# Kernel optimization log

Hardware: AMD Instinct MI355X
Metric: run time of the kernel (lower is better)

Reference implementation:

```python
import jax, jax.numpy as jnp
import numpy as np

B, S, D, F_INT = 8, 1024, 1024, 4096
N_EDGES = 262144
NUM_REL = 2
LN_EPS = 1e-6


def setup_inputs() -> dict:
    key = jax.random.key(0)
    ks = jax.random.split(key, 10)
    N = B * S
    glorot_w = float(np.sqrt(6.0 / (D + F_INT)))
    glorot_r = float(np.sqrt(6.0 / (D + F_INT)))
    return {
        "hidden_states": jax.random.normal(ks[0], (B, S, D), dtype=jnp.float32),
        "weight": jax.random.uniform(ks[1], (NUM_REL, D, F_INT), jnp.float32, -glorot_w, glorot_w),
        "root": jax.random.uniform(ks[2], (D, F_INT), jnp.float32, -glorot_r, glorot_r),
        "bias": jnp.zeros((F_INT,), jnp.float32),
        "wo": jax.random.normal(ks[3], (F_INT, D), dtype=jnp.float32) * 0.02,
        "ln_gamma": jnp.ones((D,), jnp.float32),
        "ln_beta": jnp.zeros((D,), jnp.float32),
        "edge_index": jax.random.randint(ks[4], (2, N_EDGES), 0, N, dtype=jnp.int32),
        "edge_type": jax.random.randint(ks[5], (N_EDGES,), 0, NUM_REL, dtype=jnp.int32),
    }


def reference(hidden_states, weight, root, bias, wo, ln_gamma, ln_beta, edge_index, edge_type):
    Bz, Sq, Dm = hidden_states.shape
    N = Bz * Sq
    # LayerNorm
    mu = hidden_states.mean(-1, keepdims=True)
    var = jnp.mean((hidden_states - mu) ** 2, axis=-1, keepdims=True)
    norm_x = (hidden_states - mu) * jax.lax.rsqrt(var + LN_EPS) * ln_gamma + ln_beta
    x = norm_x.reshape(N, Dm)  # [N, D] node features

    src, dst = edge_index[0], edge_index[1]
    out = jnp.zeros((N, weight.shape[2]), dtype=x.dtype)
    # RGCNConv: per-relation masked gather -> scatter-mean -> matmul
    for r in range(NUM_REL):
        mask = (edge_type == r)
        msg = jnp.where(mask[:, None], x[src], 0.0)          # [E, D]
        agg = jax.ops.segment_sum(msg, dst, num_segments=N)  # [N, D]
        cnt = jax.ops.segment_sum(mask.astype(x.dtype), dst, num_segments=N)
        h = agg / jnp.maximum(cnt, 1.0)[:, None]             # mean aggr (0 if no edges)
        out = out + h @ weight[r]
    out = out + x @ root + bias
    # relu -> wo -> residual (dropout = identity at eval)
    out = jax.nn.relu(out) @ wo
    return hidden_states + out.reshape(Bz, Sq, Dm)
```

## Files before the change

kernel.cpp:

```cpp
#include <hip/hip_runtime.h>


typedef unsigned short u16;
typedef unsigned int   u32;
typedef __attribute__((ext_vector_type(8))) short bf16x8;
typedef __attribute__((ext_vector_type(4))) float f32x4;
typedef __attribute__((ext_vector_type(2))) float f32x2;

#define E_NUM  262144
#define NNODE  8192
#define NBKT   (2 * NNODE)
#define DDIM   1024
#define FDIM   4096
#define KCAT   3072
#define LN_EPS 1e-6f

struct alignas(8) u16x4 { u16 x, y, z, w; };

__device__ __forceinline__ u16 f2bf(float f) {
  u32 u = __float_as_uint(f);
  u32 r = u + 0x7fffu + ((u >> 16) & 1u);
  return (u16)(r >> 16);
}
__device__ __forceinline__ float bf2f(u16 h) {
  return __uint_as_float(((u32)h) << 16);
}

__device__ __forceinline__ u32 enc_fp8_1(float f) {
  u32 u = __float_as_uint(f);
  u32 s = u >> 31;
  u32 mag = u & 0x7fffffffu;
  mag = mag + 0x7ffffu + ((mag >> 20) & 1u);
  if (mag > 0x43e00000u) mag = 0x43e00000u;
  u32 e = mag >> 23;
  return (e <= 120u) ? 0u
                     : ((s << 7) | ((e - 120u) << 3) | ((mag >> 20) & 7u));
}

__device__ __forceinline__ u32 pack4_fp8(float a, float b, float c, float d) {
#if __has_builtin(__builtin_amdgcn_cvt_pk_fp8_f32)
  int v = 0;
  v = __builtin_amdgcn_cvt_pk_fp8_f32(a, b, v, false);
  v = __builtin_amdgcn_cvt_pk_fp8_f32(c, d, v, true);
  return (u32)v;
#else
  return enc_fp8_1(a) | (enc_fp8_1(b) << 8) | (enc_fp8_1(c) << 16) |
         (enc_fp8_1(d) << 24);
#endif
}

__device__ __forceinline__ float dec_fp8_1(u32 b) {
  u32 e = (b >> 3) & 15u;
  u32 f = ((b & 0x80u) << 24) | ((e + 120u) << 23) | ((b & 7u) << 20);
  return e ? __uint_as_float(f) : 0.0f;
}

__device__ __forceinline__ void acc4_fp8(float* a, u32 q) {
#if __has_builtin(__builtin_amdgcn_cvt_pk_f32_fp8)
  f32x2 p0 = __builtin_amdgcn_cvt_pk_f32_fp8((int)q, false);
  f32x2 p1 = __builtin_amdgcn_cvt_pk_f32_fp8((int)q, true);
  a[0] += p0.x; a[1] += p0.y; a[2] += p1.x; a[3] += p1.y;
#else
  a[0] += dec_fp8_1(q);       a[1] += dec_fp8_1(q >> 8);
  a[2] += dec_fp8_1(q >> 16); a[3] += dec_fp8_1(q >> 24);
#endif
}

#define GLD16(gp, lp)                                              \
  __builtin_amdgcn_global_load_lds(                                \
      (__attribute__((address_space(1))) u32*)(gp),                \
      (__attribute__((address_space(3))) u32*)(lp), 16, 0, 0)

__global__ void ln_kernel(const float* __restrict__ hs,
                          const float* __restrict__ gamma,
                          const float* __restrict__ beta,
                          u16* __restrict__ hcat,
                          u32* __restrict__ xq) {
  const int row = blockIdx.x;
  const int tid = threadIdx.x;
  const float4 v = ((const float4*)(hs + (size_t)row * DDIM))[tid];

  __shared__ float r1[256], r2[256];
  r1[tid] = v.x + v.y + v.z + v.w;
  r2[tid] = v.x * v.x + v.y * v.y + v.z * v.z + v.w * v.w;
  __syncthreads();
  for (int st = 128; st > 0; st >>= 1) {
    if (tid < st) { r1[tid] += r1[tid + st]; r2[tid] += r2[tid + st]; }
    __syncthreads();
  }
  const float mean = r1[0] * (1.0f / DDIM);
  const float var  = r2[0] * (1.0f / DDIM) - mean * mean;
  const float rs   = rsqrtf(var + LN_EPS);

  const int base = tid * 4;
  const float4 g = *(const float4*)(gamma + base);
  const float4 b = *(const float4*)(beta + base);
  const float o0 = (v.x - mean) * rs * g.x + b.x;
  const float o1 = (v.y - mean) * rs * g.y + b.y;
  const float o2 = (v.z - mean) * rs * g.z + b.z;
  const float o3 = (v.w - mean) * rs * g.w + b.w;
  u16x4 o;
  o.x = f2bf(o0); o.y = f2bf(o1); o.z = f2bf(o2); o.w = f2bf(o3);
  *(u16x4*)(hcat + (size_t)row * KCAT + 2048 + base) = o;
  xq[row * 256 + tid] = pack4_fp8(o0, o1, o2, o3);
}

__global__ void cvt_transpose(const float* __restrict__ srcA,
                              const float* __restrict__ srcB,
                              int splitK, int K, int N,
                              u16* __restrict__ dst) {
  __shared__ float tile[32][33];
  const int n0 = blockIdx.x * 32, k0 = blockIdx.y * 32;
  const int tx = threadIdx.x, ty = threadIdx.y;
  for (int i = ty; i < 32; i += 8) {
    const int k = k0 + i;
    const float v = (k < splitK) ? srcA[(size_t)k * N + n0 + tx]
                                 : srcB[(size_t)(k - splitK) * N + n0 + tx];
    tile[i][tx] = v;
  }
  __syncthreads();
  for (int i = ty; i < 32; i += 8) {
    dst[(size_t)(n0 + i) * K + k0 + tx] = f2bf(tile[tx][i]);
  }
}

__global__ void count_kernel(const int* __restrict__ edge_index,
                             const int* __restrict__ edge_type,
                             int* __restrict__ cnt) {
  const int e = blockIdx.x * 256 + threadIdx.x;
  const int d = edge_index[E_NUM + e];
  const int r = edge_type[e];
  atomicAdd(&cnt[r * NNODE + d], 1);
}

__global__ __launch_bounds__(1024) void scan_kernel(const int* __restrict__ cnt,
                                                    int* __restrict__ off,
                                                    int* __restrict__ cursor) {
  __shared__ int partial[1024];
  const int tid  = threadIdx.x;
  const int base = tid * 16;
  int local[16];
  int s = 0;
#pragma unroll
  for (int i = 0; i < 16; ++i) { local[i] = s; s += cnt[base + i]; }
  partial[tid] = s;
  __syncthreads();
  for (int st = 1; st < 1024; st <<= 1) {
    const int v = (tid >= st) ? partial[tid - st] : 0;
    __syncthreads();
    partial[tid] += v;
    __syncthreads();
  }
  const int pre = (tid == 0) ? 0 : partial[tid - 1];
#pragma unroll
  for (int i = 0; i < 16; ++i) {
    const int o = pre + local[i];
    off[base + i]    = o;
    cursor[base + i] = o;
  }
}

__global__ void fill_kernel(const int* __restrict__ edge_index,
                            const int* __restrict__ edge_type,
                            int* __restrict__ cursor,
                            int* __restrict__ bucket_src) {
  const int e = blockIdx.x * 256 + threadIdx.x;
  const int s = edge_index[e];
  const int d = edge_index[E_NUM + e];
  const int r = edge_type[e];
  const int pos = atomicAdd(&cursor[r * NNODE + d], 1);
  bucket_src[pos] = s;
}

__global__ __launch_bounds__(256) void aggregate_kernel(
    const int* __restrict__ cnt, const int* __restrict__ off,
    const int* __restrict__ bucket_src, const u32* __restrict__ xq,
    u16* __restrict__ hcat) {
  const int b    = blockIdx.x;
  const int r    = b >> 13;
  const int node = b & (NNODE - 1);
  const int tid  = threadIdx.x;
  const int g    = tid >> 6;
  const int c    = tid & 63;
  const int n     = cnt[b];
  const int start = off[b];

  __shared__ int   ids[256];
  __shared__ float red[3 * 1024];
  float a[16] = {};

  for (int c0 = 0; c0 < n; c0 += 256) {
    const int m = min(n - c0, 256);
    __syncthreads();
    if (tid < m) ids[tid] = bucket_src[start + c0 + tid];
    __syncthreads();
    int j = g;
    for (; j + 4 < m; j += 8) {
      const int s0 = ids[j], s1 = ids[j + 4];
      const uint4 x0 = *(const uint4*)(xq + s0 * 256 + c * 4);
      const uint4 x1 = *(const uint4*)(xq + s1 * 256 + c * 4);
      acc4_fp8(a + 0,  x0.x); acc4_fp8(a + 4,  x0.y);
      acc4_fp8(a + 8,  x0.z); acc4_fp8(a + 12, x0.w);
      acc4_fp8(a + 0,  x1.x); acc4_fp8(a + 4,  x1.y);
      acc4_fp8(a + 8,  x1.z); acc4_fp8(a + 12, x1.w);
    }
    for (; j < m; j += 4) {
      const int s0 = ids[j];
      const uint4 x0 = *(const uint4*)(xq + s0 * 256 + c * 4);
      acc4_fp8(a + 0,  x0.x); acc4_fp8(a + 4,  x0.y);
      acc4_fp8(a + 8,  x0.z); acc4_fp8(a + 12, x0.w);
    }
  }

  if (g != 0) {
    float* d = red + (g - 1) * 1024 + c * 16;
#pragma unroll
    for (int i = 0; i < 4; ++i)
      *(float4*)(d + i * 4) = make_float4(a[i*4+0], a[i*4+1], a[i*4+2], a[i*4+3]);
  }
  __syncthreads();
  if (g == 0) {
#pragma unroll
    for (int k = 0; k < 3; ++k) {
      const float* d = red + k * 1024 + c * 16;
#pragma unroll
      for (int i = 0; i < 16; ++i) a[i] += d[i];
    }
    const float inv = 1.0f / fmaxf((float)n, 1.0f);
    uint4 o0, o1;
    o0.x = (u32)f2bf(a[0] * inv)  | ((u32)f2bf(a[1] * inv)  << 16);
    o0.y = (u32)f2bf(a[2] * inv)  | ((u32)f2bf(a[3] * inv)  << 16);
    o0.z = (u32)f2bf(a[4] * inv)  | ((u32)f2bf(a[5] * inv)  << 16);
    o0.w = (u32)f2bf(a[6] * inv)  | ((u32)f2bf(a[7] * inv)  << 16);
    o1.x = (u32)f2bf(a[8] * inv)  | ((u32)f2bf(a[9] * inv)  << 16);
    o1.y = (u32)f2bf(a[10] * inv) | ((u32)f2bf(a[11] * inv) << 16);
    o1.z = (u32)f2bf(a[12] * inv) | ((u32)f2bf(a[13] * inv) << 16);
    o1.w = (u32)f2bf(a[14] * inv) | ((u32)f2bf(a[15] * inv) << 16);
    u16* dp = hcat + (size_t)node * KCAT + (size_t)r * DDIM + c * 16;
    *(uint4*)(dp)     = o0;
    *(uint4*)(dp + 8) = o1;
  }
}


#define MF16(a, b, c) __builtin_amdgcn_mfma_f32_16x16x32_bf16(a, b, c, 0, 0, 0)

#define STAGE_A(t, p, b)                                                   \
  { GLD16(gA0 + (size_t)(t) * 64 + (size_t)(p) * KP,                       \
          &sA[b][(p) * 8192 + lofs0]);                                     \
    GLD16(gA1 + (size_t)(t) * 64 + (size_t)(p) * KP,                       \
          &sA[b][(p) * 8192 + lofs1]); }

#define STAGE_B(t, p, b)                                                   \
  { GLD16(gB0 + (size_t)(t) * 64 + (size_t)(p) * KP,                       \
          &sB[b][(p) * 8192 + lofs0]);                                     \
    GLD16(gB1 + (size_t)(t) * 64 + (size_t)(p) * KP,                       \
          &sB[b][(p) * 8192 + lofs1]); }

#define BVLOAD(b)                                                          \
  { const bf16x8* pB_ = (const bf16x8*)sB[b];                              \
    bv[0][0] = pB_[brow80 + sega0]; bv[0][1] = pB_[brow80 + sega1];        \
    bv[1][0] = pB_[brow81 + sega0]; bv[1][1] = pB_[brow81 + sega1];        \
    bv[2][0] = pB_[brow82 + sega0]; bv[2][1] = pB_[brow82 + sega1];        \
    bv[3][0] = pB_[brow83 + sega0]; bv[3][1] = pB_[brow83 + sega1]; }

#define NOWAIT ((void)0)
#define NOSTAGE ((void)0)
#define VM4 asm volatile("s_waitcnt vmcnt(4)" ::: "memory")
#define VM2 asm volatile("s_waitcnt vmcnt(2)" ::: "memory")
#define VM0 asm volatile("s_waitcnt vmcnt(0)" ::: "memory")

#define PHASE(Q, BUFI, STAGE, ENDW)                                        \
  { const bf16x8* pA_ = (const bf16x8*)sA[BUFI];                           \
    bf16x8 a00 = pA_[arow8[2 * (Q)] + sega0];                              \
    bf16x8 a01 = pA_[arow8[2 * (Q)] + sega1];                              \
    bf16x8 a10 = pA_[arow8[2 * (Q) + 1] + sega0];                          \
    bf16x8 a11 = pA_[arow8[2 * (Q) + 1] + sega1];                          \
    STAGE;                                                                 \
    __builtin_amdgcn_s_barrier();                                          \
    asm volatile("s_waitcnt lgkmcnt(0)" ::: "memory");                     \
    __builtin_amdgcn_s_setprio(1);                                         \
    _Pragma("unroll")                                                      \
    for (int ni = 0; ni < 4; ++ni) {                                       \
      acc[2 * (Q)][ni]     = MF16(a00, bv[ni][0], acc[2 * (Q)][ni]);       \
      acc[2 * (Q)][ni]     = MF16(a01, bv[ni][1], acc[2 * (Q)][ni]);       \
      acc[2 * (Q) + 1][ni] = MF16(a10, bv[ni][0], acc[2 * (Q) + 1][ni]);   \
      acc[2 * (Q) + 1][ni] = MF16(a11, bv[ni][1], acc[2 * (Q) + 1][ni]);   \
    }                                                                      \
    __builtin_amdgcn_s_setprio(0);                                         \
    ENDW;                                                                  \
    __builtin_amdgcn_s_barrier(); }

__global__ __launch_bounds__(512) void gemm1_kernel(
    const u16* __restrict__ A, const u16* __restrict__ Bt,
    const float* __restrict__ bias, u16* __restrict__ obf) {
  const int K = KCAT, N = FDIM;
  const int NT = K / 64;
  const size_t KP = (size_t)128 * K;
  __shared__ __align__(16) u16 sA[2][16384];
  __shared__ __align__(16) u16 sB[2][16384];

  const int tid  = threadIdx.x;
  const int lane = tid & 63;
  const int wave = tid >> 6;
  const int wr = wave >> 2, wc = wave & 3;
  const int lr = lane & 15, quad = lane >> 4;

  const int bid = blockIdx.x;
  const int swz = (bid & 7) * 64 + (bid >> 3);
  const int bm = (swz >> 4) * 256;
  const int bn = (swz & 15) * 256;

  int lofs0, lofs1;
  const u16 *gA0, *gA1, *gB0, *gB1;
  {
    const int s0 = tid,       r0 = s0 >> 3, g0 = (s0 & 7) ^ (r0 & 7);
    const int s1 = tid + 512, r1 = s1 >> 3, g1 = (s1 & 7) ^ (r1 & 7);
    gA0 = A  + (size_t)(bm + r0) * K + g0 * 8;
    gA1 = A  + (size_t)(bm + r1) * K + g1 * 8;
    gB0 = Bt + (size_t)(bn + r0) * K + g0 * 8;
    gB1 = Bt + (size_t)(bn + r1) * K + g1 * 8;
    lofs0 = s0 * 8; lofs1 = s1 * 8;
  }

  int arow8[8];
#pragma unroll
  for (int mi = 0; mi < 8; ++mi) arow8[mi] = (wr * 128 + mi * 16 + lr) * 8;
  const int brow80 = (wc * 64 +  0 + lr) * 8;
  const int brow81 = (wc * 64 + 16 + lr) * 8;
  const int brow82 = (wc * 64 + 32 + lr) * 8;
  const int brow83 = (wc * 64 + 48 + lr) * 8;
  const int sega0 = quad ^ (lr & 7);
  const int sega1 = (4 + quad) ^ (lr & 7);

  f32x4 acc[8][4] = {};
  bf16x8 bv[4][2];

  STAGE_B(0, 0, 0) STAGE_B(0, 1, 0)
  STAGE_A(0, 0, 0) STAGE_A(0, 1, 0)
  STAGE_B(1, 0, 1) STAGE_B(1, 1, 1)
  asm volatile("s_waitcnt vmcnt(4)" ::: "memory");
  __builtin_amdgcn_s_barrier();

  for (int tt = 0; tt < NT - 2; tt += 2) {
    PHASE(0, 0, BVLOAD(0); STAGE_A(tt + 1, 0, 1), NOWAIT)
    PHASE(1, 0, STAGE_A(tt + 1, 1, 1), NOWAIT)
    PHASE(2, 0, STAGE_B(tt + 2, 0, 0), NOWAIT)
    PHASE(3, 0, STAGE_B(tt + 2, 1, 0), VM4)
    PHASE(0, 1, BVLOAD(1); STAGE_A(tt + 2, 0, 0), NOWAIT)
    PHASE(1, 1, STAGE_A(tt + 2, 1, 0), NOWAIT)
    PHASE(2, 1, STAGE_B(tt + 3, 0, 1), NOWAIT)
    PHASE(3, 1, STAGE_B(tt + 3, 1, 1), VM4)
  }
  PHASE(0, 0, BVLOAD(0); STAGE_A(NT - 1, 0, 1), NOWAIT)
  PHASE(1, 0, STAGE_A(NT - 1, 1, 1), NOWAIT)
  PHASE(2, 0, NOSTAGE, NOWAIT)
  PHASE(3, 0, NOSTAGE, VM0)
  PHASE(0, 1, BVLOAD(1), NOWAIT)
  PHASE(1, 1, NOSTAGE, NOWAIT)
  PHASE(2, 1, NOSTAGE, NOWAIT)
  PHASE(3, 1, NOSTAGE, NOWAIT)

#pragma unroll
  for (int mi = 0; mi < 8; ++mi) {
#pragma unroll
    for (int ni = 0; ni < 4; ++ni) {
      const int col  = bn + wc * 64 + ni * 16 + lr;
      const int row0 = bm + wr * 128 + mi * 16 + quad * 4;
      const float bb = bias[col];
#pragma unroll
      for (int r = 0; r < 4; ++r) {
        float v = acc[mi][ni][r] + bb;
        v = fmaxf(v, 0.0f);
        obf[(size_t)(row0 + r) * N + col] = f2bf(v);
      }
    }
  }
}

__global__ __launch_bounds__(512) void gemm2_kernel(
    const u16* __restrict__ A, const u16* __restrict__ Bt,
    const float* __restrict__ resid, float* __restrict__ out) {
  const int K = FDIM, N = DDIM;
  const int NT = K / 64;
  const size_t KP = (size_t)128 * K;
  __shared__ __align__(16) u16 sA[2][16384];
  __shared__ __align__(16) u16 sB[2][8192];

  const int tid  = threadIdx.x;
  const int lane = tid & 63;
  const int wave = tid >> 6;
  const int wr = wave >> 1, wc = wave & 1;
  const int lr = lane & 15, quad = lane >> 4;

  const int bid = blockIdx.x;
  const int swz = (bid & 7) * 32 + (bid >> 3);
  const int bm = (swz >> 3) * 256;
  const int bn = (swz & 7) * 128;

  int lofs0, lofs1;
  const u16 *gA0, *gA1, *gB0, *gB1;
  {
    const int s0 = tid,       r0 = s0 >> 3, g0 = (s0 & 7) ^ (r0 & 7);
    const int s1 = tid + 512, r1 = s1 >> 3, g1 = (s1 & 7) ^ (r1 & 7);
    gA0 = A  + (size_t)(bm + r0) * K + g0 * 8;
    gA1 = A  + (size_t)(bm + r1) * K + g1 * 8;
    gB0 = Bt + (size_t)(bn + r0) * K + g0 * 8;
    gB1 = Bt + (size_t)(bn + r1) * K + g1 * 8;
    lofs0 = s0 * 8; lofs1 = s1 * 8;
  }

  int arow8[4];
#pragma unroll
  for (int mi = 0; mi < 4; ++mi) arow8[mi] = (wr * 64 + mi * 16 + lr) * 8;
  const int brow80 = (wc * 64 +  0 + lr) * 8;
  const int brow81 = (wc * 64 + 16 + lr) * 8;
  const int brow82 = (wc * 64 + 32 + lr) * 8;
  const int brow83 = (wc * 64 + 48 + lr) * 8;
  const int sega0 = quad ^ (lr & 7);
  const int sega1 = (4 + quad) ^ (lr & 7);

  f32x4 acc[4][4] = {};
  bf16x8 bv[4][2];

  STAGE_B(0, 0, 0)
  STAGE_A(0, 0, 0) STAGE_A(0, 1, 0)
  STAGE_B(1, 0, 1)
  asm volatile("s_waitcnt vmcnt(2)" ::: "memory");
  __builtin_amdgcn_s_barrier();

  for (int tt = 0; tt < NT - 2; tt += 2) {
    PHASE(0, 0, BVLOAD(0); STAGE_A(tt + 1, 0, 1), NOWAIT)
    PHASE(1, 0, STAGE_A(tt + 1, 1, 1); STAGE_B(tt + 2, 0, 0), VM2)
    PHASE(0, 1, BVLOAD(1); STAGE_A(tt + 2, 0, 0), NOWAIT)
    PHASE(1, 1, STAGE_A(tt + 2, 1, 0); STAGE_B(tt + 3, 0, 1), VM2)
  }
  PHASE(0, 0, BVLOAD(0); STAGE_A(NT - 1, 0, 1), NOWAIT)
  PHASE(1, 0, STAGE_A(NT - 1, 1, 1), VM0)
  PHASE(0, 1, BVLOAD(1), NOWAIT)
  PHASE(1, 1, NOSTAGE, NOWAIT)

#pragma unroll
  for (int mi = 0; mi < 4; ++mi) {
#pragma unroll
    for (int ni = 0; ni < 4; ++ni) {
      const int col  = bn + wc * 64 + ni * 16 + lr;
      const int row0 = bm + wr * 64 + mi * 16 + quad * 4;
#pragma unroll
      for (int r = 0; r < 4; ++r) {
        const size_t idx = (size_t)(row0 + r) * N + col;
        out[idx] = resid[idx] + acc[mi][ni][r];
      }
    }
  }
}

extern "C" void kernel_launch(void* const* d_in, const int* in_sizes, int n_in,
                              void* d_out, int out_size, void* d_ws, size_t ws_size,
                              hipStream_t stream) {
  const float* hs     = (const float*)d_in[0];
  const float* weight = (const float*)d_in[1];
  const float* root   = (const float*)d_in[2];
  const float* bias   = (const float*)d_in[3];
  const float* wo     = (const float*)d_in[4];
  const float* gamma  = (const float*)d_in[5];
  const float* beta   = (const float*)d_in[6];
  const int* edge_index = (const int*)d_in[7];
  const int* edge_type  = (const int*)d_in[8];
  float* out = (float*)d_out;

  char* ws = (char*)d_ws;
  u16*   hcat       = (u16*)(ws + 0);
  u16*   WcatT      = (u16*)(ws + 50331648);
  u16*   woT        = (u16*)(ws + 75497472);
  u16*   out1       = (u16*)(ws + 83886080);
  int*   bucket_src = (int*)(ws + 83886080);
  int*   cnt        = (int*)(ws + 84934656);
  int*   off        = (int*)(ws + 85000192);
  int*   cursor     = (int*)(ws + 85065728);
  u32*   xq         = (u32*)(ws + 85131264);

  (void)hipMemsetAsync(cnt, 0, 65536, stream);

  ln_kernel<<<NNODE, 256, 0, stream>>>(hs, gamma, beta, hcat, xq);

  cvt_transpose<<<dim3(FDIM / 32, KCAT / 32), dim3(32, 8), 0, stream>>>(
      weight, root, 2048, KCAT, FDIM, WcatT);
  cvt_transpose<<<dim3(DDIM / 32, FDIM / 32), dim3(32, 8), 0, stream>>>(
      wo, wo, FDIM, FDIM, DDIM, woT);

  count_kernel<<<E_NUM / 256, 256, 0, stream>>>(edge_index, edge_type, cnt);
  scan_kernel<<<1, 1024, 0, stream>>>(cnt, off, cursor);
  fill_kernel<<<E_NUM / 256, 256, 0, stream>>>(edge_index, edge_type, cursor, bucket_src);
  aggregate_kernel<<<NBKT, 256, 0, stream>>>(cnt, off, bucket_src, xq, hcat);

  gemm1_kernel<<<512, 512, 0, stream>>>(hcat, WcatT, bias, out1);

  gemm2_kernel<<<256, 512, 0, stream>>>(out1, woT, hs, out);
}
```

Baseline: 474.5 us.

## Use one wavefront per bucket in aggregation and double-buffer A fragments in GEMM1

The aggregation kernel now gives each (relation, node) bucket to a single 64-lane wavefront, four buckets per block. Source ids are broadcast with shuffles instead of staged through LDS, which removes the shared-memory cross-wave reduction and its syncthreads. Separately, the GEMM1 main loop now uses two register banks of A fragments and prefetches the next phase's A reads after the barrier, ahead of the current MFMAs, with sched_barrier and setprio fencing. The intent is to hide LDS read latency behind matrix math. In exchange, register pressure rises and aggregation parallelism per bucket falls, since there are fewer lanes per node.

```diff
diff --git a/kernel.cpp b/kernel.cpp
--- a/kernel.cpp
+++ b/kernel.cpp
@@ -64,6 +64,11 @@
   a[0] += dec_fp8_1(q);       a[1] += dec_fp8_1(q >> 8);
   a[2] += dec_fp8_1(q >> 16); a[3] += dec_fp8_1(q >> 24);
 #endif
+}
+
+__device__ __forceinline__ void acc16_fp8(float* a, uint4 x) {
+  acc4_fp8(a + 0,  x.x); acc4_fp8(a + 4,  x.y);
+  acc4_fp8(a + 8,  x.z); acc4_fp8(a + 12, x.w);
 }
 
 #define GLD16(gp, lp)                                              \
@@ -176,70 +181,51 @@
     const int* __restrict__ cnt, const int* __restrict__ off,
     const int* __restrict__ bucket_src, const u32* __restrict__ xq,
     u16* __restrict__ hcat) {
-  const int b    = blockIdx.x;
+  const int b    = blockIdx.x * 4 + (threadIdx.x >> 6);
+  const int lane = threadIdx.x & 63;
   const int r    = b >> 13;
   const int node = b & (NNODE - 1);
-  const int tid  = threadIdx.x;
-  const int g    = tid >> 6;
-  const int c    = tid & 63;
   const int n     = cnt[b];
   const int start = off[b];
 
-  __shared__ int   ids[256];
-  __shared__ float red[3 * 1024];
   float a[16] = {};
 
-  for (int c0 = 0; c0 < n; c0 += 256) {
-    const int m = min(n - c0, 256);
-    __syncthreads();
-    if (tid < m) ids[tid] = bucket_src[start + c0 + tid];
-    __syncthreads();
-    int j = g;
-    for (; j + 4 < m; j += 8) {
-      const int s0 = ids[j], s1 = ids[j + 4];
-      const uint4 x0 = *(const uint4*)(xq + s0 * 256 + c * 4);
-      const uint4 x1 = *(const uint4*)(xq + s1 * 256 + c * 4);
-      acc4_fp8(a + 0,  x0.x); acc4_fp8(a + 4,  x0.y);
-      acc4_fp8(a + 8,  x0.z); acc4_fp8(a + 12, x0.w);
-      acc4_fp8(a + 0,  x1.x); acc4_fp8(a + 4,  x1.y);
-      acc4_fp8(a + 8,  x1.z); acc4_fp8(a + 12, x1.w);
+  for (int j0 = 0; j0 < n; j0 += 64) {
+    const int m = min(n - j0, 64);
+    const int myid = (lane < m) ? bucket_src[start + j0 + lane] : 0;
+    int j = 0;
+    for (; j + 3 < m; j += 4) {
+      const int s0 = __shfl(myid, j,     64);
+      const int s1 = __shfl(myid, j + 1, 64);
+      const int s2 = __shfl(myid, j + 2, 64);
+      const int s3 = __shfl(myid, j + 3, 64);
+      const uint4 x0 = *(const uint4*)(xq + s0 * 256 + lane * 4);
+      const uint4 x1 = *(const uint4*)(xq + s1 * 256 + lane * 4);
+      const uint4 x2 = *(const uint4*)(xq + s2 * 256 + lane * 4);
+      const uint4 x3 = *(const uint4*)(xq + s3 * 256 + lane * 4);
+      acc16_fp8(a, x0); acc16_fp8(a, x1);
+      acc16_fp8(a, x2); acc16_fp8(a, x3);
     }
-    for (; j < m; j += 4) {
-      const int s0 = ids[j];
-      const uint4 x0 = *(const uint4*)(xq + s0 * 256 + c * 4);
-      acc4_fp8(a + 0,  x0.x); acc4_fp8(a + 4,  x0.y);
-      acc4_fp8(a + 8,  x0.z); acc4_fp8(a + 12, x0.w);
+    for (; j < m; ++j) {
+      const int s0 = __shfl(myid, j, 64);
+      const uint4 x0 = *(const uint4*)(xq + s0 * 256 + lane * 4);
+      acc16_fp8(a, x0);
     }
   }
 
-  if (g != 0) {
-    float* d = red + (g - 1) * 1024 + c * 16;
-#pragma unroll
-    for (int i = 0; i < 4; ++i)
-      *(float4*)(d + i * 4) = make_float4(a[i*4+0], a[i*4+1], a[i*4+2], a[i*4+3]);
-  }
-  __syncthreads();
-  if (g == 0) {
-#pragma unroll
-    for (int k = 0; k < 3; ++k) {
-      const float* d = red + k * 1024 + c * 16;
-#pragma unroll
-      for (int i = 0; i < 16; ++i) a[i] += d[i];
-    }
-    const float inv = 1.0f / fmaxf((float)n, 1.0f);
-    uint4 o0, o1;
-    o0.x = (u32)f2bf(a[0] * inv)  | ((u32)f2bf(a[1] * inv)  << 16);
-    o0.y = (u32)f2bf(a[2] * inv)  | ((u32)f2bf(a[3] * inv)  << 16);
-    o0.z = (u32)f2bf(a[4] * inv)  | ((u32)f2bf(a[5] * inv)  << 16);
-    o0.w = (u32)f2bf(a[6] * inv)  | ((u32)f2bf(a[7] * inv)  << 16);
-    o1.x = (u32)f2bf(a[8] * inv)  | ((u32)f2bf(a[9] * inv)  << 16);
-    o1.y = (u32)f2bf(a[10] * inv) | ((u32)f2bf(a[11] * inv) << 16);
-    o1.z = (u32)f2bf(a[12] * inv) | ((u32)f2bf(a[13] * inv) << 16);
-    o1.w = (u32)f2bf(a[14] * inv) | ((u32)f2bf(a[15] * inv) << 16);
-    u16* dp = hcat + (size_t)node * KCAT + (size_t)r * DDIM + c * 16;
-    *(uint4*)(dp)     = o0;
-    *(uint4*)(dp + 8) = o1;
-  }
+  const float inv = 1.0f / fmaxf((float)n, 1.0f);
+  uint4 o0, o1;
+  o0.x = (u32)f2bf(a[0] * inv)  | ((u32)f2bf(a[1] * inv)  << 16);
+  o0.y = (u32)f2bf(a[2] * inv)  | ((u32)f2bf(a[3] * inv)  << 16);
+  o0.z = (u32)f2bf(a[4] * inv)  | ((u32)f2bf(a[5] * inv)  << 16);
+  o0.w = (u32)f2bf(a[6] * inv)  | ((u32)f2bf(a[7] * inv)  << 16);
+  o1.x = (u32)f2bf(a[8] * inv)  | ((u32)f2bf(a[9] * inv)  << 16);
+  o1.y = (u32)f2bf(a[10] * inv) | ((u32)f2bf(a[11] * inv) << 16);
+  o1.z = (u32)f2bf(a[12] * inv) | ((u32)f2bf(a[13] * inv) << 16);
+  o1.w = (u32)f2bf(a[14] * inv) | ((u32)f2bf(a[15] * inv) << 16);
+  u16* dp = hcat + (size_t)node * KCAT + (size_t)r * DDIM + lane * 16;
+  *(uint4*)(dp)     = o0;
+  *(uint4*)(dp + 8) = o1;
 }
 
 
@@ -266,9 +252,39 @@
 
 #define NOWAIT ((void)0)
 #define NOSTAGE ((void)0)
+#define NOOP ((void)0)
 #define VM4 asm volatile("s_waitcnt vmcnt(4)" ::: "memory")
 #define VM2 asm volatile("s_waitcnt vmcnt(2)" ::: "memory")
 #define VM0 asm volatile("s_waitcnt vmcnt(0)" ::: "memory")
+
+#define AREAD(BANK, Q, BUFI)                                               \
+  { const bf16x8* pA_ = (const bf16x8*)sA[BUFI];                           \
+    af##BANK##0 = pA_[arow8[2 * (Q)] + sega0];                             \
+    af##BANK##1 = pA_[arow8[2 * (Q)] + sega1];                             \
+    af##BANK##2 = pA_[arow8[2 * (Q) + 1] + sega0];                         \
+    af##BANK##3 = pA_[arow8[2 * (Q) + 1] + sega1]; }
+
+#define AMFMA(BANK, Q)                                                     \
+    _Pragma("unroll")                                                      \
+    for (int ni = 0; ni < 4; ++ni) {                                       \
+      acc[2 * (Q)][ni]     = MF16(af##BANK##0, bv[ni][0], acc[2 * (Q)][ni]);\
+      acc[2 * (Q)][ni]     = MF16(af##BANK##1, bv[ni][1], acc[2 * (Q)][ni]);\
+      acc[2 * (Q) + 1][ni] = MF16(af##BANK##2, bv[ni][0], acc[2 * (Q) + 1][ni]);\
+      acc[2 * (Q) + 1][ni] = MF16(af##BANK##3, bv[ni][1], acc[2 * (Q) + 1][ni]);\
+    }
+
+#define PHX(Q, BANK, OWN, PRE, STAGE, ENDW)                                \
+  { OWN;                                                                   \
+    STAGE;                                                                 \
+    __builtin_amdgcn_s_barrier();                                          \
+    asm volatile("s_waitcnt lgkmcnt(0)" ::: "memory");                     \
+    PRE;                                                                   \
+    __builtin_amdgcn_sched_barrier(0);                                     \
+    __builtin_amdgcn_s_setprio(1);                                         \
+    AMFMA(BANK, Q)                                                         \
+    __builtin_amdgcn_s_setprio(0);                                         \
+    ENDW;                                                                  \
+    __builtin_amdgcn_s_barrier(); }
 
 #define PHASE(Q, BUFI, STAGE, ENDW)                                        \
   { const bf16x8* pA_ = (const bf16x8*)sA[BUFI];                           \
@@ -335,6 +351,8 @@
 
   f32x4 acc[8][4] = {};
   bf16x8 bv[4][2];
+  bf16x8 af00, af01, af02, af03;
+  bf16x8 af10, af11, af12, af13;
 
   STAGE_B(0, 0, 0) STAGE_B(0, 1, 0)
   STAGE_A(0, 0, 0) STAGE_A(0, 1, 0)
@@ -343,23 +361,23 @@
   __builtin_amdgcn_s_barrier();
 
   for (int tt = 0; tt < NT - 2; tt += 2) {
-    PHASE(0, 0, BVLOAD(0); STAGE_A(tt + 1, 0, 1), NOWAIT)
-    PHASE(1, 0, STAGE_A(tt + 1, 1, 1), NOWAIT)
-    PHASE(2, 0, STAGE_B(tt + 2, 0, 0), NOWAIT)
-    PHASE(3, 0, STAGE_B(tt + 2, 1, 0), VM4)
-    PHASE(0, 1, BVLOAD(1); STAGE_A(tt + 2, 0, 0), NOWAIT)
-    PHASE(1, 1, STAGE_A(tt + 2, 1, 0), NOWAIT)
-    PHASE(2, 1, STAGE_B(tt + 3, 0, 1), NOWAIT)
-    PHASE(3, 1, STAGE_B(tt + 3, 1, 1), VM4)
-  }
-  PHASE(0, 0, BVLOAD(0); STAGE_A(NT - 1, 0, 1), NOWAIT)
-  PHASE(1, 0, STAGE_A(NT - 1, 1, 1), NOWAIT)
-  PHASE(2, 0, NOSTAGE, NOWAIT)
-  PHASE(3, 0, NOSTAGE, VM0)
-  PHASE(0, 1, BVLOAD(1), NOWAIT)
-  PHASE(1, 1, NOSTAGE, NOWAIT)
-  PHASE(2, 1, NOSTAGE, NOWAIT)
-  PHASE(3, 1, NOSTAGE, NOWAIT)
+    PHX(0, 0, AREAD(0, 0, 0); BVLOAD(0), AREAD(1, 1, 0), STAGE_A(tt + 1, 0, 1), NOWAIT)
+    PHX(1, 1, NOOP,                      AREAD(0, 2, 0), STAGE_A(tt + 1, 1, 1), NOWAIT)
+    PHX(2, 0, NOOP,                      AREAD(1, 3, 0), STAGE_B(tt + 2, 0, 0), NOWAIT)
+    PHX(3, 1, NOOP,                      NOOP,           STAGE_B(tt + 2, 1, 0), VM4)
+    PHX(0, 0, AREAD(0, 0, 1); BVLOAD(1), AREAD(1, 1, 1), STAGE_A(tt + 2, 0, 0), NOWAIT)
+    PHX(1, 1, NOOP,                      AREAD(0, 2, 1), STAGE_A(tt + 2, 1, 0), NOWAIT)
+    PHX(2, 0, NOOP,                      AREAD(1, 3, 1), STAGE_B(tt + 3, 0, 1), NOWAIT)
+    PHX(3, 1, NOOP,                      NOOP,           STAGE_B(tt + 3, 1, 1), VM4)
+  }
+  PHX(0, 0, AREAD(0, 0, 0); BVLOAD(0), AREAD(1, 1, 0), STAGE_A(NT - 1, 0, 1), NOWAIT)
+  PHX(1, 1, NOOP,                      AREAD(0, 2, 0), STAGE_A(NT - 1, 1, 1), NOWAIT)
+  PHX(2, 0, NOOP,                      AREAD(1, 3, 0), NOSTAGE, NOWAIT)
+  PHX(3, 1, NOOP,                      NOOP,           NOSTAGE, VM0)
+  PHX(0, 0, AREAD(0, 0, 1); BVLOAD(1), AREAD(1, 1, 1), NOSTAGE, NOWAIT)
+  PHX(1, 1, NOOP,                      AREAD(0, 2, 1), NOSTAGE, NOWAIT)
+  PHX(2, 0, NOOP,                      AREAD(1, 3, 1), NOSTAGE, NOWAIT)
+  PHX(3, 1, NOOP,                      NOOP,           NOSTAGE, NOWAIT)
 
 #pragma unroll
   for (int mi = 0; mi < 8; ++mi) {
@@ -492,7 +510,7 @@
   count_kernel<<<E_NUM / 256, 256, 0, stream>>>(edge_index, edge_type, cnt);
   scan_kernel<<<1, 1024, 0, stream>>>(cnt, off, cursor);
   fill_kernel<<<E_NUM / 256, 256, 0, stream>>>(edge_index, edge_type, cursor, bucket_src);
-  aggregate_kernel<<<NBKT, 256, 0, stream>>>(cnt, off, bucket_src, xq, hcat);
+  aggregate_kernel<<<NBKT / 4, 256, 0, stream>>>(cnt, off, bucket_src, xq, hcat);
 
   gemm1_kernel<<<512, 512, 0, stream>>>(hcat, WcatT, bias, out1);
 
```

Result: no change. 483.3 us (+1.9%).

## Fuse edge counting into LayerNorm, use wave-per-bucket aggregation, stage GEMM1 epilogue via LDS

Applied to the files above, without the earlier changes.

The edge-count atomics now run inside the LayerNorm kernel, so the separate count kernel is gone. Aggregation maps one wavefront to each (relation, node) bucket and broadcasts source ids with shuffles. This removes the LDS id staging, the cross-wave reduction and the block barriers. The GEMM1 epilogue writes bias+ReLU bf16 results into reused shared memory, then emits coalesced 16-byte row stores instead of scattered 2-byte stores. It adds two extra barriers per half tile, and each bucket's gather now runs on a single wave.

```diff
diff --git a/kernel.cpp b/kernel.cpp
--- a/kernel.cpp
+++ b/kernel.cpp
@@ -66,6 +66,11 @@
 #endif
 }
 
+__device__ __forceinline__ void acc16_fp8(float* a, uint4 x) {
+  acc4_fp8(a + 0,  x.x); acc4_fp8(a + 4,  x.y);
+  acc4_fp8(a + 8,  x.z); acc4_fp8(a + 12, x.w);
+}
+
 #define GLD16(gp, lp)                                              \
   __builtin_amdgcn_global_load_lds(                                \
       (__attribute__((address_space(1))) u32*)(gp),                \
@@ -75,10 +80,20 @@
                           const float* __restrict__ gamma,
                           const float* __restrict__ beta,
                           u16* __restrict__ hcat,
-                          u32* __restrict__ xq) {
+                          u32* __restrict__ xq,
+                          const int* __restrict__ edge_index,
+                          const int* __restrict__ edge_type,
+                          int* __restrict__ cnt) {
   const int row = blockIdx.x;
   const int tid = threadIdx.x;
   const float4 v = ((const float4*)(hs + (size_t)row * DDIM))[tid];
+
+  if (tid < 32) {
+    const int e = (row << 5) + tid;
+    const int d = edge_index[E_NUM + e];
+    const int r = edge_type[e];
+    atomicAdd(&cnt[r * NNODE + d], 1);
+  }
 
   __shared__ float r1[256], r2[256];
   r1[tid] = v.x + v.y + v.z + v.w;
@@ -124,15 +139,6 @@
   }
 }
 
-__global__ void count_kernel(const int* __restrict__ edge_index,
-                             const int* __restrict__ edge_type,
-                             int* __restrict__ cnt) {
-  const int e = blockIdx.x * 256 + threadIdx.x;
-  const int d = edge_index[E_NUM + e];
-  const int r = edge_type[e];
-  atomicAdd(&cnt[r * NNODE + d], 1);
-}
-
 __global__ __launch_bounds__(1024) void scan_kernel(const int* __restrict__ cnt,
                                                     int* __restrict__ off,
                                                     int* __restrict__ cursor) {
@@ -176,70 +182,51 @@
     const int* __restrict__ cnt, const int* __restrict__ off,
     const int* __restrict__ bucket_src, const u32* __restrict__ xq,
     u16* __restrict__ hcat) {
-  const int b    = blockIdx.x;
+  const int b    = blockIdx.x * 4 + (threadIdx.x >> 6);
+  const int lane = threadIdx.x & 63;
   const int r    = b >> 13;
   const int node = b & (NNODE - 1);
-  const int tid  = threadIdx.x;
-  const int g    = tid >> 6;
-  const int c    = tid & 63;
   const int n     = cnt[b];
   const int start = off[b];
 
-  __shared__ int   ids[256];
-  __shared__ float red[3 * 1024];
   float a[16] = {};
 
-  for (int c0 = 0; c0 < n; c0 += 256) {
-    const int m = min(n - c0, 256);
-    __syncthreads();
-    if (tid < m) ids[tid] = bucket_src[start + c0 + tid];
-    __syncthreads();
-    int j = g;
-    for (; j + 4 < m; j += 8) {
-      const int s0 = ids[j], s1 = ids[j + 4];
-      const uint4 x0 = *(const uint4*)(xq + s0 * 256 + c * 4);
-      const uint4 x1 = *(const uint4*)(xq + s1 * 256 + c * 4);
-      acc4_fp8(a + 0,  x0.x); acc4_fp8(a + 4,  x0.y);
-      acc4_fp8(a + 8,  x0.z); acc4_fp8(a + 12, x0.w);
-      acc4_fp8(a + 0,  x1.x); acc4_fp8(a + 4,  x1.y);
-      acc4_fp8(a + 8,  x1.z); acc4_fp8(a + 12, x1.w);
+  for (int j0 = 0; j0 < n; j0 += 64) {
+    const int m = min(n - j0, 64);
+    const int myid = (lane < m) ? bucket_src[start + j0 + lane] : 0;
+    int j = 0;
+    for (; j + 3 < m; j += 4) {
+      const int s0 = __shfl(myid, j,     64);
+      const int s1 = __shfl(myid, j + 1, 64);
+      const int s2 = __shfl(myid, j + 2, 64);
+      const int s3 = __shfl(myid, j + 3, 64);
+      const uint4 x0 = *(const uint4*)(xq + s0 * 256 + lane * 4);
+      const uint4 x1 = *(const uint4*)(xq + s1 * 256 + lane * 4);
+      const uint4 x2 = *(const uint4*)(xq + s2 * 256 + lane * 4);
+      const uint4 x3 = *(const uint4*)(xq + s3 * 256 + lane * 4);
+      acc16_fp8(a, x0); acc16_fp8(a, x1);
+      acc16_fp8(a, x2); acc16_fp8(a, x3);
     }
-    for (; j < m; j += 4) {
-      const int s0 = ids[j];
-      const uint4 x0 = *(const uint4*)(xq + s0 * 256 + c * 4);
-      acc4_fp8(a + 0,  x0.x); acc4_fp8(a + 4,  x0.y);
-      acc4_fp8(a + 8,  x0.z); acc4_fp8(a + 12, x0.w);
+    for (; j < m; ++j) {
+      const int s0 = __shfl(myid, j, 64);
+      const uint4 x0 = *(const uint4*)(xq + s0 * 256 + lane * 4);
+      acc16_fp8(a, x0);
     }
   }
 
-  if (g != 0) {
-    float* d = red + (g - 1) * 1024 + c * 16;
-#pragma unroll
-    for (int i = 0; i < 4; ++i)
-      *(float4*)(d + i * 4) = make_float4(a[i*4+0], a[i*4+1], a[i*4+2], a[i*4+3]);
-  }
-  __syncthreads();
-  if (g == 0) {
-#pragma unroll
-    for (int k = 0; k < 3; ++k) {
-      const float* d = red + k * 1024 + c * 16;
-#pragma unroll
-      for (int i = 0; i < 16; ++i) a[i] += d[i];
-    }
-    const float inv = 1.0f / fmaxf((float)n, 1.0f);
-    uint4 o0, o1;
-    o0.x = (u32)f2bf(a[0] * inv)  | ((u32)f2bf(a[1] * inv)  << 16);
-    o0.y = (u32)f2bf(a[2] * inv)  | ((u32)f2bf(a[3] * inv)  << 16);
-    o0.z = (u32)f2bf(a[4] * inv)  | ((u32)f2bf(a[5] * inv)  << 16);
-    o0.w = (u32)f2bf(a[6] * inv)  | ((u32)f2bf(a[7] * inv)  << 16);
-    o1.x = (u32)f2bf(a[8] * inv)  | ((u32)f2bf(a[9] * inv)  << 16);
-    o1.y = (u32)f2bf(a[10] * inv) | ((u32)f2bf(a[11] * inv) << 16);
-    o1.z = (u32)f2bf(a[12] * inv) | ((u32)f2bf(a[13] * inv) << 16);
-    o1.w = (u32)f2bf(a[14] * inv) | ((u32)f2bf(a[15] * inv) << 16);
-    u16* dp = hcat + (size_t)node * KCAT + (size_t)r * DDIM + c * 16;
-    *(uint4*)(dp)     = o0;
-    *(uint4*)(dp + 8) = o1;
-  }
+  const float inv = 1.0f / fmaxf((float)n, 1.0f);
+  uint4 o0, o1;
+  o0.x = (u32)f2bf(a[0] * inv)  | ((u32)f2bf(a[1] * inv)  << 16);
+  o0.y = (u32)f2bf(a[2] * inv)  | ((u32)f2bf(a[3] * inv)  << 16);
+  o0.z = (u32)f2bf(a[4] * inv)  | ((u32)f2bf(a[5] * inv)  << 16);
+  o0.w = (u32)f2bf(a[6] * inv)  | ((u32)f2bf(a[7] * inv)  << 16);
+  o1.x = (u32)f2bf(a[8] * inv)  | ((u32)f2bf(a[9] * inv)  << 16);
+  o1.y = (u32)f2bf(a[10] * inv) | ((u32)f2bf(a[11] * inv) << 16);
+  o1.z = (u32)f2bf(a[12] * inv) | ((u32)f2bf(a[13] * inv) << 16);
+  o1.w = (u32)f2bf(a[14] * inv) | ((u32)f2bf(a[15] * inv) << 16);
+  u16* dp = hcat + (size_t)node * KCAT + (size_t)r * DDIM + lane * 16;
+  *(uint4*)(dp)     = o0;
+  *(uint4*)(dp + 8) = o1;
 }
 
 
@@ -297,8 +284,9 @@
   const int K = KCAT, N = FDIM;
   const int NT = K / 64;
   const size_t KP = (size_t)128 * K;
-  __shared__ __align__(16) u16 sA[2][16384];
-  __shared__ __align__(16) u16 sB[2][16384];
+  __shared__ __align__(16) u16 smem[65536];
+  u16 (*sA)[16384] = (u16(*)[16384])(smem);
+  u16 (*sB)[16384] = (u16(*)[16384])(smem + 32768);
 
   const int tid  = threadIdx.x;
   const int lane = tid & 63;
@@ -361,20 +349,35 @@
   PHASE(2, 1, NOSTAGE, NOWAIT)
   PHASE(3, 1, NOSTAGE, NOWAIT)
 
-#pragma unroll
-  for (int mi = 0; mi < 8; ++mi) {
-#pragma unroll
-    for (int ni = 0; ni < 4; ++ni) {
-      const int col  = bn + wc * 64 + ni * 16 + lr;
-      const int row0 = bm + wr * 128 + mi * 16 + quad * 4;
-      const float bb = bias[col];
-#pragma unroll
-      for (int r = 0; r < 4; ++r) {
-        float v = acc[mi][ni][r] + bb;
-        v = fmaxf(v, 0.0f);
-        obf[(size_t)(row0 + r) * N + col] = f2bf(v);
+  const int CPAD = 264;
+#pragma unroll
+  for (int h = 0; h < 2; ++h) {
+    if (wr == h) {
+#pragma unroll
+      for (int mi = 0; mi < 8; ++mi) {
+        const int lrow = mi * 16 + quad * 4;
+#pragma unroll
+        for (int ni = 0; ni < 4; ++ni) {
+          const int col = wc * 64 + ni * 16 + lr;
+          const float bb = bias[bn + col];
+#pragma unroll
+          for (int r = 0; r < 4; ++r) {
+            const float v = acc[mi][ni][r] + bb;
+            smem[(lrow + r) * CPAD + col] = f2bf(fmaxf(v, 0.0f));
+          }
+        }
       }
     }
+    __syncthreads();
+#pragma unroll
+    for (int i = 0; i < 8; ++i) {
+      const int chunk = tid + 512 * i;
+      const int row = chunk >> 5;
+      const int seg = chunk & 31;
+      const uint4 val = *(const uint4*)(smem + row * CPAD + seg * 8);
+      *(uint4*)(obf + (size_t)(bm + h * 128 + row) * N + bn + seg * 8) = val;
+    }
+    __syncthreads();
   }
 }
 
@@ -482,18 +485,18 @@
 
   (void)hipMemsetAsync(cnt, 0, 65536, stream);
 
-  ln_kernel<<<NNODE, 256, 0, stream>>>(hs, gamma, beta, hcat, xq);
+  ln_kernel<<<NNODE, 256, 0, stream>>>(hs, gamma, beta, hcat, xq,
+                                       edge_index, edge_type, cnt);
+
+  scan_kernel<<<1, 1024, 0, stream>>>(cnt, off, cursor);
+  fill_kernel<<<E_NUM / 256, 256, 0, stream>>>(edge_index, edge_type, cursor, bucket_src);
+  aggregate_kernel<<<NBKT / 4, 256, 0, stream>>>(cnt, off, bucket_src, xq, hcat);
 
   cvt_transpose<<<dim3(FDIM / 32, KCAT / 32), dim3(32, 8), 0, stream>>>(
       weight, root, 2048, KCAT, FDIM, WcatT);
   cvt_transpose<<<dim3(DDIM / 32, FDIM / 32), dim3(32, 8), 0, stream>>>(
       wo, wo, FDIM, FDIM, DDIM, woT);
 
-  count_kernel<<<E_NUM / 256, 256, 0, stream>>>(edge_index, edge_type, cnt);
-  scan_kernel<<<1, 1024, 0, stream>>>(cnt, off, cursor);
-  fill_kernel<<<E_NUM / 256, 256, 0, stream>>>(edge_index, edge_type, cursor, bucket_src);
-  aggregate_kernel<<<NBKT, 256, 0, stream>>>(cnt, off, bucket_src, xq, hcat);
-
   gemm1_kernel<<<512, 512, 0, stream>>>(hcat, WcatT, bias, out1);
 
   gemm2_kernel<<<256, 512, 0, stream>>>(out1, woT, hs, out);
```

Result: no change. 475.3 us (+0.2%).
